# Optimization experiments

Hardware: AMD Instinct MI355X
Metric: run time of the kernel (lower is better)

## Reference

```python
import jax, jax.numpy as jnp
import numpy as np

DT = 0.01
DT_SCALE = 1.0

B, D, R = 4096, 1024, 256

def setup_inputs() -> dict:
    key = jax.random.key(0)
    kx, kv, kf, ku, kw = jax.random.split(key, 5)
    x = jax.random.normal(kx, (B, D), dtype=jnp.float32)
    v = jax.random.normal(kv, (B, D), dtype=jnp.float32)
    force = jax.random.normal(kf, (B, D), dtype=jnp.float32)
    # low-rank Christoffel factors; scaled down so the quadratic term stays stable
    U = jax.random.normal(ku, (D, R), dtype=jnp.float32) * (1.0 / np.sqrt(D))
    W = jax.random.normal(kw, (R, D), dtype=jnp.float32) * (1.0 / np.sqrt(R))
    return {"x": x, "v": v, "force": force, "U": U, "W": W, "steps": 8}

def christoffel(v, U, W):
    # Gamma(v, v) = ((v @ U) ** 2) @ W  -- factored quadratic form
    p = v @ U            # [B, R]
    return (p * p) @ W   # [B, D]

def reference(x, v, force, U, W, steps):
    dt = DT * DT_SCALE

    def step(carry, _):
        cx, cv = carry
        acc = force - christoffel(cv, U, W)
        cx = cx + dt * cv
        cv = cv + dt * acc
        return (cx, cv), None

    (cx, cv), _ = jax.lax.scan(step, (x, v), None, length=steps)
    return (cx, cv)
```

## Files before the change

kernel.cpp:

```cpp
#include <hip/hip_runtime.h>


#define BB 4096
#define DD 1024
#define RR 256
#define DT 0.01f

typedef __attribute__((ext_vector_type(8))) short short8;
typedef __attribute__((ext_vector_type(4))) short short4v;
typedef __attribute__((ext_vector_type(4))) float floatx4;

static __device__ inline unsigned short f2bf(float f) {
    union { float f; unsigned int u; } c; c.f = f;
    unsigned int u = c.u;
    u += 0x7fffu + ((u >> 16) & 1u);
    return (unsigned short)(u >> 16);
}

__global__ __launch_bounds__(1024)
void pack_kernel(const float* __restrict__ U, const float* __restrict__ W,
                 short* __restrict__ Up, short* __restrict__ Wp,
                 short* __restrict__ WUp) {
    __shared__ float4 red[16][64];
    const int b = blockIdx.x;
    const int tid = threadIdx.x;

    if (b < 128) {
        const bool isU = (b < 64);
        const float* M = isU ? U : W;
        short* P = isU ? Up : Wp;
        const int ld = isU ? RR : DD;
        int t = (isU ? b : b - 64) * 1024 + tid;
        int S = t * 4;
        int j0   = S & 7;
        int lane = (S >> 3) & 63;
        int frag = S >> 9;
        int nl = lane & 15, kq = lane >> 4;
        int kt, nt;
        if (isU) { kt = frag >> 4; nt = frag & 15; }
        else     { kt = frag >> 6; nt = frag & 63; }
        int k0 = kt * 32 + kq * 8 + j0;
        int n  = nt * 16 + nl;
        short4v o;
#pragma unroll
        for (int jj = 0; jj < 4; jj++)
            o[jj] = (short)f2bf(M[(long)(k0 + jj) * ld + n]);
        *(short4v*)(P + S) = o;
    } else {
        const int i  = b - 128;
        const int ks = tid >> 6;
        const int j4 = tid & 63;
        const float4* U4 = (const float4*)U;
        const float*  wr = W + (long)i * DD + ks * 64;
        float4 acc = {0.f, 0.f, 0.f, 0.f};
#pragma unroll 8
        for (int m = 0; m < 64; m++) {
            float w = wr[m];
            float4 u = U4[(ks * 64 + m) * 64 + j4];
            acc.x += w * u.x; acc.y += w * u.y;
            acc.z += w * u.z; acc.w += w * u.w;
        }
        red[ks][j4] = acc;
        __syncthreads();
        if (tid < 64) {
            float4 a = red[0][tid];
#pragma unroll
            for (int s = 1; s < 16; s++) {
                float4 r = red[s][tid];
                a.x += r.x; a.y += r.y; a.z += r.z; a.w += r.w;
            }
            int ktw = i >> 5, kqw = (i >> 3) & 3, jjw = i & 7;
            float av[4] = {a.x, a.y, a.z, a.w};
#pragma unroll
            for (int c = 0; c < 4; c++) {
                int j = 4 * tid + c;
                int nt = j >> 4, nl = j & 15;
                WUp[(((ktw * 16 + nt) * 64) + kqw * 16 + nl) * 8 + jjw] =
                    (short)f2bf(av[c]);
            }
        }
    }
}

__global__ __launch_bounds__(1024, 8)
void euler_kernel(const float* __restrict__ x0,
                  const float* __restrict__ v0,
                  const float* __restrict__ force,
                  const short8* __restrict__ Up,
                  const short8* __restrict__ Wp,
                  const short8* __restrict__ WUp,
                  const int* __restrict__ steps_p,
                  float* __restrict__ out) {
    __shared__ __align__(16) short smem[32768];

    const int tid  = threadIdx.x;
    const int wave = tid >> 6;
    const int lane = tid & 63;
    const int nl   = lane & 15;
    const int quad = lane >> 4;
    const int row0 = blockIdx.x * 8;
    const int steps = steps_p[0];

    short (*va)[1032] = (short(*)[1032])smem;
    short (*fa)[1032] = (short(*)[1032])(smem + 8256);
    short (*q1)[264]  = (short(*)[264])(smem + 16512);
    short (*q2)[264]  = (short(*)[264])(smem + 20736);

    const float4* v04 = (const float4*)v0;
    const float4* f44 = (const float4*)force;
#pragma unroll
    for (int i = 0; i < 2; i++) {
        int idx = tid + i * 1024;
        int row = idx >> 8, c4 = idx & 255;
        long g = (long)(row0 + row) * 256 + c4;
        float4 vv = v04[g];
        float4 ff = f44[g];
        short4v sv, sf;
        sv[0] = (short)f2bf(vv.x); sv[1] = (short)f2bf(vv.y);
        sv[2] = (short)f2bf(vv.z); sv[3] = (short)f2bf(vv.w);
        sf[0] = (short)f2bf(ff.x); sf[1] = (short)f2bf(ff.y);
        sf[2] = (short)f2bf(ff.z); sf[3] = (short)f2bf(ff.w);
        *(short4v*)&va[row][c4 * 4] = sv;
        *(short4v*)&fa[row][c4 * 4] = sf;
    }
    __syncthreads();

    floatx4 P  = {0.f, 0.f, 0.f, 0.f};
    floatx4 FU = {0.f, 0.f, 0.f, 0.f};
#pragma unroll 4
    for (int kt = 0; kt < 32; kt++) {
        short8 av = *(const short8*)&va[nl][kt * 32 + quad * 8];
        short8 af = *(const short8*)&fa[nl][kt * 32 + quad * 8];
        short8 bu = Up[(kt * 16 + wave) * 64 + lane];
        P  = __builtin_amdgcn_mfma_f32_16x16x32_bf16(av, bu, P,  0, 0, 0);
        FU = __builtin_amdgcn_mfma_f32_16x16x32_bf16(af, bu, FU, 0, 0, 0);
    }

    short8 wu[8];
#pragma unroll
    for (int kt = 0; kt < 8; kt++)
        wu[kt] = WUp[(kt * 16 + wave) * 64 + lane];

    floatx4 A1 = {0.f, 0.f, 0.f, 0.f};
    floatx4 Q2 = {0.f, 0.f, 0.f, 0.f};
    for (int s = 0; s < steps; s++) {
        short (*pw)[264] = (s & 1) ? q2 : q1;
        float wgt = (float)(steps - 1 - s);
#pragma unroll
        for (int r = 0; r < 4; r++) {
            float g = P[r] * P[r];
            A1[r] += g;
            Q2[r] += wgt * g;
            pw[4 * quad + r][16 * wave + nl] = (short)f2bf(g);
        }
        __syncthreads();
        floatx4 acc = {0.f, 0.f, 0.f, 0.f};
#pragma unroll
        for (int kt = 0; kt < 8; kt++) {
            short8 a = *(const short8*)&pw[nl][kt * 32 + quad * 8];
            acc = __builtin_amdgcn_mfma_f32_16x16x32_bf16(a, wu[kt], acc, 0, 0, 0);
        }
#pragma unroll
        for (int r = 0; r < 4; r++)
            P[r] += DT * (FU[r] - acc[r]);
    }
    __syncthreads();

#pragma unroll
    for (int r = 0; r < 4; r++) {
        q1[4 * quad + r][16 * wave + nl] = (short)f2bf(A1[r]);
        q2[4 * quad + r][16 * wave + nl] = (short)f2bf(Q2[r]);
    }
    __syncthreads();

    floatx4 y1[4], y2[4];
#pragma unroll
    for (int t = 0; t < 4; t++) {
        y1[t] = (floatx4){0.f, 0.f, 0.f, 0.f};
        y2[t] = (floatx4){0.f, 0.f, 0.f, 0.f};
    }
#pragma unroll 2
    for (int kt = 0; kt < 8; kt++) {
        short8 a1 = *(const short8*)&q1[nl][kt * 32 + quad * 8];
        short8 a2 = *(const short8*)&q2[nl][kt * 32 + quad * 8];
#pragma unroll
        for (int t = 0; t < 4; t++) {
            short8 b = Wp[(kt * 64 + 4 * wave + t) * 64 + lane];
            y1[t] = __builtin_amdgcn_mfma_f32_16x16x32_bf16(a1, b, y1[t], 0, 0, 0);
            y2[t] = __builtin_amdgcn_mfma_f32_16x16x32_bf16(a2, b, y2[t], 0, 0, 0);
        }
    }
    __syncthreads();

    float (*s1)[1024] = (float(*)[1024])smem;
    float (*s2)[1024] = (float(*)[1024])(smem + 16384);
    if (quad < 2) {
#pragma unroll
        for (int t = 0; t < 4; t++) {
            int col = 64 * wave + 16 * t + nl;
#pragma unroll
            for (int r = 0; r < 4; r++) {
                int row = 4 * quad + r;
                s1[row][col] = -DT * y1[t][r];
                s2[row][col] = -DT * DT * y2[t][r];
            }
        }
    }
    __syncthreads();

    const float sdt  = steps * DT;
    const float tdt2 = 0.5f * (float)(steps * (steps - 1)) * DT * DT;
    const float4* x4 = (const float4*)x0;
    float4* out4 = (float4*)out;
#pragma unroll
    for (int p = 0; p < 2; p++) {
        int idx = tid + p * 1024;
        int row = idx >> 8, c4 = idx & 255;
        long gi = (long)(row0 + row) * 256 + c4;
        float4 xx = x4[gi];
        float4 vv = v04[gi];
        float4 ff = f44[gi];
        float4 t1 = *(const float4*)&s1[row][c4 * 4];
        float4 t2 = *(const float4*)&s2[row][c4 * 4];
        float4 ox, ov;
        ox.x = xx.x + sdt * vv.x + tdt2 * ff.x + t2.x;
        ox.y = xx.y + sdt * vv.y + tdt2 * ff.y + t2.y;
        ox.z = xx.z + sdt * vv.z + tdt2 * ff.z + t2.z;
        ox.w = xx.w + sdt * vv.w + tdt2 * ff.w + t2.w;
        ov.x = vv.x + sdt * ff.x + t1.x;
        ov.y = vv.y + sdt * ff.y + t1.y;
        ov.z = vv.z + sdt * ff.z + t1.z;
        ov.w = vv.w + sdt * ff.w + t1.w;
        out4[gi] = ox;
        out4[(long)BB * 256 + gi] = ov;
    }
}

extern "C" void kernel_launch(void* const* d_in, const int* in_sizes, int n_in,
                              void* d_out, int out_size, void* d_ws, size_t ws_size,
                              hipStream_t stream) {
    const float* x     = (const float*)d_in[0];
    const float* v     = (const float*)d_in[1];
    const float* force = (const float*)d_in[2];
    const float* U     = (const float*)d_in[3];
    const float* W     = (const float*)d_in[4];
    const int*   steps = (const int*)d_in[5];

    short* Up  = (short*)d_ws;
    short* Wp  = Up + 262144;
    short* WUp = Wp + 262144;

    pack_kernel<<<384, 1024, 0, stream>>>(U, W, Up, Wp, WUp);
    euler_kernel<<<512, 1024, 0, stream>>>(x, v, force,
                                           (const short8*)Up, (const short8*)Wp,
                                           (const short8*)WUp,
                                           steps, (float*)d_out);
}
```

Before: 179.3 us.

## Halve block size to 512 threads, each wave handling two column tiles

Shrinks the euler block from 1024 to 512 threads, with each wave computing two 16-column tiles of the projection and recurrence. Shared memory drops by removing the separate force buffer: force and v are converted and projected one after another through a single staging buffer. The step loop uses a single q buffer with an extra barrier per step instead of double buffering. The output stage writes x and v results in two passes through one fp32 staging area. The aim is lower LDS use and higher occupancy, at the cost of more registers per thread, more barriers and a second pass over Up.

Measured after the change: 177.4 us. No clear change (-1.1%).

```diff
diff --git a/kernel.cpp b/kernel.cpp
--- a/kernel.cpp
+++ b/kernel.cpp
@@ -82,7 +82,7 @@
     }
 }
 
-__global__ __launch_bounds__(1024, 8)
+__global__ __launch_bounds__(512, 4)
 void euler_kernel(const float* __restrict__ x0,
                   const float* __restrict__ v0,
                   const float* __restrict__ force,
@@ -91,148 +91,182 @@
                   const short8* __restrict__ WUp,
                   const int* __restrict__ steps_p,
                   float* __restrict__ out) {
-    __shared__ __align__(16) short smem[32768];
+    __shared__ __align__(16) short smem[24960];
 
     const int tid  = threadIdx.x;
-    const int wave = tid >> 6;
+    const int w    = tid >> 6;
     const int lane = tid & 63;
     const int nl   = lane & 15;
     const int quad = lane >> 4;
     const int row0 = blockIdx.x * 8;
     const int steps = steps_p[0];
+    const float sdt  = steps * DT;
+    const float tdt2 = 0.5f * (float)(steps * (steps - 1)) * DT * DT;
 
     short (*va)[1032] = (short(*)[1032])smem;
-    short (*fa)[1032] = (short(*)[1032])(smem + 8256);
     short (*q1)[264]  = (short(*)[264])(smem + 16512);
     short (*q2)[264]  = (short(*)[264])(smem + 20736);
 
     const float4* v04 = (const float4*)v0;
     const float4* f44 = (const float4*)force;
-#pragma unroll
-    for (int i = 0; i < 2; i++) {
-        int idx = tid + i * 1024;
+    const float4* x4  = (const float4*)x0;
+
+    {
+        unsigned* z = (unsigned*)smem;
+        for (int i = tid; i < 4128; i += 512) z[4128 + i] = 0u;
+    }
+    float4 vv[4];
+#pragma unroll
+    for (int p = 0; p < 4; p++) {
+        int idx = tid + p * 512;
         int row = idx >> 8, c4 = idx & 255;
         long g = (long)(row0 + row) * 256 + c4;
-        float4 vv = v04[g];
         float4 ff = f44[g];
-        short4v sv, sf;
-        sv[0] = (short)f2bf(vv.x); sv[1] = (short)f2bf(vv.y);
-        sv[2] = (short)f2bf(vv.z); sv[3] = (short)f2bf(vv.w);
+        vv[p] = v04[g];
+        short4v sf;
         sf[0] = (short)f2bf(ff.x); sf[1] = (short)f2bf(ff.y);
         sf[2] = (short)f2bf(ff.z); sf[3] = (short)f2bf(ff.w);
-        *(short4v*)&va[row][c4 * 4] = sv;
-        *(short4v*)&fa[row][c4 * 4] = sf;
-    }
-    __syncthreads();
-
-    floatx4 P  = {0.f, 0.f, 0.f, 0.f};
-    floatx4 FU = {0.f, 0.f, 0.f, 0.f};
+        *(short4v*)&va[row][c4 * 4] = sf;
+    }
+    __syncthreads();
+
+    floatx4 FU0 = {0.f,0.f,0.f,0.f}, FU1 = {0.f,0.f,0.f,0.f};
 #pragma unroll 4
     for (int kt = 0; kt < 32; kt++) {
-        short8 av = *(const short8*)&va[nl][kt * 32 + quad * 8];
-        short8 af = *(const short8*)&fa[nl][kt * 32 + quad * 8];
-        short8 bu = Up[(kt * 16 + wave) * 64 + lane];
-        P  = __builtin_amdgcn_mfma_f32_16x16x32_bf16(av, bu, P,  0, 0, 0);
-        FU = __builtin_amdgcn_mfma_f32_16x16x32_bf16(af, bu, FU, 0, 0, 0);
-    }
-
-    short8 wu[8];
-#pragma unroll
-    for (int kt = 0; kt < 8; kt++)
-        wu[kt] = WUp[(kt * 16 + wave) * 64 + lane];
-
-    floatx4 A1 = {0.f, 0.f, 0.f, 0.f};
-    floatx4 Q2 = {0.f, 0.f, 0.f, 0.f};
+        short8 a  = *(const short8*)&va[nl][kt * 32 + quad * 8];
+        short8 b0 = Up[(kt * 16 + w) * 64 + lane];
+        short8 b1 = Up[(kt * 16 + w + 8) * 64 + lane];
+        FU0 = __builtin_amdgcn_mfma_f32_16x16x32_bf16(a, b0, FU0, 0, 0, 0);
+        FU1 = __builtin_amdgcn_mfma_f32_16x16x32_bf16(a, b1, FU1, 0, 0, 0);
+    }
+    __syncthreads();
+
+#pragma unroll
+    for (int p = 0; p < 4; p++) {
+        int idx = tid + p * 512;
+        int row = idx >> 8, c4 = idx & 255;
+        short4v sv;
+        sv[0] = (short)f2bf(vv[p].x); sv[1] = (short)f2bf(vv[p].y);
+        sv[2] = (short)f2bf(vv[p].z); sv[3] = (short)f2bf(vv[p].w);
+        *(short4v*)&va[row][c4 * 4] = sv;
+    }
+    __syncthreads();
+
+    short8 wu0[8], wu1[8];
+#pragma unroll
+    for (int kt = 0; kt < 8; kt++) {
+        wu0[kt] = WUp[(kt * 16 + w) * 64 + lane];
+        wu1[kt] = WUp[(kt * 16 + w + 8) * 64 + lane];
+    }
+
+    floatx4 P0 = {0.f,0.f,0.f,0.f}, P1 = {0.f,0.f,0.f,0.f};
+#pragma unroll 4
+    for (int kt = 0; kt < 32; kt++) {
+        short8 a  = *(const short8*)&va[nl][kt * 32 + quad * 8];
+        short8 b0 = Up[(kt * 16 + w) * 64 + lane];
+        short8 b1 = Up[(kt * 16 + w + 8) * 64 + lane];
+        P0 = __builtin_amdgcn_mfma_f32_16x16x32_bf16(a, b0, P0, 0, 0, 0);
+        P1 = __builtin_amdgcn_mfma_f32_16x16x32_bf16(a, b1, P1, 0, 0, 0);
+    }
+
+    floatx4 A10 = {0.f,0.f,0.f,0.f}, A11 = {0.f,0.f,0.f,0.f};
+    floatx4 Q20 = {0.f,0.f,0.f,0.f}, Q21 = {0.f,0.f,0.f,0.f};
     for (int s = 0; s < steps; s++) {
-        short (*pw)[264] = (s & 1) ? q2 : q1;
         float wgt = (float)(steps - 1 - s);
 #pragma unroll
         for (int r = 0; r < 4; r++) {
-            float g = P[r] * P[r];
-            A1[r] += g;
-            Q2[r] += wgt * g;
-            pw[4 * quad + r][16 * wave + nl] = (short)f2bf(g);
-        }
-        __syncthreads();
-        floatx4 acc = {0.f, 0.f, 0.f, 0.f};
+            float g0 = P0[r] * P0[r];
+            float g1 = P1[r] * P1[r];
+            A10[r] += g0; Q20[r] += wgt * g0;
+            A11[r] += g1; Q21[r] += wgt * g1;
+            q1[4 * quad + r][16 * w + nl]       = (short)f2bf(g0);
+            q1[4 * quad + r][16 * (w + 8) + nl] = (short)f2bf(g1);
+        }
+        __syncthreads();
+        floatx4 acc0 = {0.f,0.f,0.f,0.f}, acc1 = {0.f,0.f,0.f,0.f};
 #pragma unroll
         for (int kt = 0; kt < 8; kt++) {
-            short8 a = *(const short8*)&pw[nl][kt * 32 + quad * 8];
-            acc = __builtin_amdgcn_mfma_f32_16x16x32_bf16(a, wu[kt], acc, 0, 0, 0);
-        }
-#pragma unroll
-        for (int r = 0; r < 4; r++)
-            P[r] += DT * (FU[r] - acc[r]);
-    }
-    __syncthreads();
+            short8 a = *(const short8*)&q1[nl][kt * 32 + quad * 8];
+            acc0 = __builtin_amdgcn_mfma_f32_16x16x32_bf16(a, wu0[kt], acc0, 0, 0, 0);
+            acc1 = __builtin_amdgcn_mfma_f32_16x16x32_bf16(a, wu1[kt], acc1, 0, 0, 0);
+        }
+#pragma unroll
+        for (int r = 0; r < 4; r++) {
+            P0[r] += DT * (FU0[r] - acc0[r]);
+            P1[r] += DT * (FU1[r] - acc1[r]);
+        }
+        __syncthreads();
+    }
 
 #pragma unroll
     for (int r = 0; r < 4; r++) {
-        q1[4 * quad + r][16 * wave + nl] = (short)f2bf(A1[r]);
-        q2[4 * quad + r][16 * wave + nl] = (short)f2bf(Q2[r]);
-    }
-    __syncthreads();
-
-    floatx4 y1[4], y2[4];
-#pragma unroll
-    for (int t = 0; t < 4; t++) {
-        y1[t] = (floatx4){0.f, 0.f, 0.f, 0.f};
-        y2[t] = (floatx4){0.f, 0.f, 0.f, 0.f};
+        q1[4 * quad + r][16 * w + nl]       = (short)f2bf(A10[r]);
+        q1[4 * quad + r][16 * (w + 8) + nl] = (short)f2bf(A11[r]);
+        q2[4 * quad + r][16 * w + nl]       = (short)f2bf(Q20[r]);
+        q2[4 * quad + r][16 * (w + 8) + nl] = (short)f2bf(Q21[r]);
+    }
+    __syncthreads();
+
+    floatx4 y1[8], y2[8];
+#pragma unroll
+    for (int t = 0; t < 8; t++) {
+        y1[t] = (floatx4){0.f,0.f,0.f,0.f};
+        y2[t] = (floatx4){0.f,0.f,0.f,0.f};
     }
 #pragma unroll 2
     for (int kt = 0; kt < 8; kt++) {
         short8 a1 = *(const short8*)&q1[nl][kt * 32 + quad * 8];
         short8 a2 = *(const short8*)&q2[nl][kt * 32 + quad * 8];
 #pragma unroll
-        for (int t = 0; t < 4; t++) {
-            short8 b = Wp[(kt * 64 + 4 * wave + t) * 64 + lane];
+        for (int t = 0; t < 8; t++) {
+            short8 b = Wp[(kt * 64 + 8 * w + t) * 64 + lane];
             y1[t] = __builtin_amdgcn_mfma_f32_16x16x32_bf16(a1, b, y1[t], 0, 0, 0);
             y2[t] = __builtin_amdgcn_mfma_f32_16x16x32_bf16(a2, b, y2[t], 0, 0, 0);
         }
     }
-    __syncthreads();
-
-    float (*s1)[1024] = (float(*)[1024])smem;
-    float (*s2)[1024] = (float(*)[1024])(smem + 16384);
-    if (quad < 2) {
-#pragma unroll
-        for (int t = 0; t < 4; t++) {
-            int col = 64 * wave + 16 * t + nl;
-#pragma unroll
-            for (int r = 0; r < 4; r++) {
-                int row = 4 * quad + r;
-                s1[row][col] = -DT * y1[t][r];
-                s2[row][col] = -DT * DT * y2[t][r];
-            }
-        }
-    }
-    __syncthreads();
-
-    const float sdt  = steps * DT;
-    const float tdt2 = 0.5f * (float)(steps * (steps - 1)) * DT * DT;
-    const float4* x4 = (const float4*)x0;
+
+    float (*sst)[1032] = (float(*)[1032])smem;
     float4* out4 = (float4*)out;
 #pragma unroll
-    for (int p = 0; p < 2; p++) {
-        int idx = tid + p * 1024;
-        int row = idx >> 8, c4 = idx & 255;
-        long gi = (long)(row0 + row) * 256 + c4;
-        float4 xx = x4[gi];
-        float4 vv = v04[gi];
-        float4 ff = f44[gi];
-        float4 t1 = *(const float4*)&s1[row][c4 * 4];
-        float4 t2 = *(const float4*)&s2[row][c4 * 4];
-        float4 ox, ov;
-        ox.x = xx.x + sdt * vv.x + tdt2 * ff.x + t2.x;
-        ox.y = xx.y + sdt * vv.y + tdt2 * ff.y + t2.y;
-        ox.z = xx.z + sdt * vv.z + tdt2 * ff.z + t2.z;
-        ox.w = xx.w + sdt * vv.w + tdt2 * ff.w + t2.w;
-        ov.x = vv.x + sdt * ff.x + t1.x;
-        ov.y = vv.y + sdt * ff.y + t1.y;
-        ov.z = vv.z + sdt * ff.z + t1.z;
-        ov.w = vv.w + sdt * ff.w + t1.w;
-        out4[gi] = ox;
-        out4[(long)BB * 256 + gi] = ov;
+    for (int sel = 0; sel < 2; sel++) {
+        if (quad < 2) {
+#pragma unroll
+            for (int t = 0; t < 8; t++) {
+                int col = 128 * w + 16 * t + nl;
+#pragma unroll
+                for (int r = 0; r < 4; r++) {
+                    int row = 4 * quad + r;
+                    sst[row][col] = sel ? (-DT * y1[t][r])
+                                        : (-DT * DT * y2[t][r]);
+                }
+            }
+        }
+        __syncthreads();
+#pragma unroll
+        for (int p = 0; p < 4; p++) {
+            int idx = tid + p * 512;
+            int row = idx >> 8, c4 = idx & 255;
+            long gi = (long)(row0 + row) * 256 + c4;
+            float4 t = *(const float4*)&sst[row][c4 * 4];
+            float4 ff = f44[gi];
+            float4 vq = v04[gi];
+            float4 o;
+            if (sel == 0) {
+                float4 xx = x4[gi];
+                o.x = xx.x + sdt * vq.x + tdt2 * ff.x + t.x;
+                o.y = xx.y + sdt * vq.y + tdt2 * ff.y + t.y;
+                o.z = xx.z + sdt * vq.z + tdt2 * ff.z + t.z;
+                o.w = xx.w + sdt * vq.w + tdt2 * ff.w + t.w;
+                out4[gi] = o;
+            } else {
+                o.x = vq.x + sdt * ff.x + t.x;
+                o.y = vq.y + sdt * ff.y + t.y;
+                o.z = vq.z + sdt * ff.z + t.z;
+                o.w = vq.w + sdt * ff.w + t.w;
+                out4[(long)BB * 256 + gi] = o;
+            }
+        }
+        __syncthreads();
     }
 }
 
@@ -251,8 +285,8 @@
     short* WUp = Wp + 262144;
 
     pack_kernel<<<384, 1024, 0, stream>>>(U, W, Up, Wp, WUp);
-    euler_kernel<<<512, 1024, 0, stream>>>(x, v, force,
-                                           (const short8*)Up, (const short8*)Wp,
-                                           (const short8*)WUp,
-                                           steps, (float*)d_out);
-}
+    euler_kernel<<<512, 512, 0, stream>>>(x, v, force,
+                                          (const short8*)Up, (const short8*)Wp,
+                                          (const short8*)WUp,
+                                          steps, (float*)d_out);
+}
```
